# Kernel optimization log

Measured on AMD Instinct MI355X. Metric: run time of the kernel, lower is better.

The kernel has to match this reference:

```python
import jax, jax.numpy as jnp
import numpy as np

N, D, T, P, NP, H = 200000, 128, 8, 2000, 9, 2048


def setup_inputs() -> dict:
    key = jax.random.key(0)
    ks = jax.random.split(key, 12)
    inp = {
        'motion_z': jax.random.normal(ks[0], (N, D), jnp.float32),
        'tasks': jax.random.randint(ks[1], (N,), 0, T, jnp.int32),
        'tasks_mask': jax.random.randint(ks[2], (N,), 0, 2, jnp.int32),
        'patient_ids': jax.random.randint(ks[3], (N,), 0, P, jnp.int32),
        'phenos': jax.random.uniform(ks[4], (N, NP), jnp.float32),
        'phenos_mask': jax.random.randint(ks[5], (N,), 0, 2, jnp.int32),
        'W1': jax.random.normal(ks[6], (T * D, H), jnp.float32) * 0.02,
        'b1': jnp.zeros((H,), jnp.float32),
        'W2': jax.random.normal(ks[7], (H, H), jnp.float32) * 0.02,
        'b2': jnp.zeros((H,), jnp.float32),
        'W3': jax.random.normal(ks[8], (H, NP), jnp.float32) * 0.02,
        'b3': jnp.zeros((NP,), jnp.float32),
    }
    return inp


def _fingerprint(motion_z, tasks, tasks_mask, patient_ids, phenos, phenos_mask):
    # valid sample mask (tasks_mask==1 & patient id present & phenos_mask==1)
    valid = (tasks_mask == 1) & (phenos_mask == 1)
    w = valid.astype(motion_z.dtype)                      # [N]
    wz = motion_z * w[:, None]                            # [N, D]

    # global per-task mean (fallback for empty patient-task cells)
    t_sum = jax.ops.segment_sum(wz, tasks, num_segments=T)           # [T, D]
    t_cnt = jax.ops.segment_sum(w, tasks, num_segments=T)            # [T]
    task_mean = t_sum / jnp.maximum(t_cnt, 1.0)[:, None]             # [T, D]

    # fused (patient, task) segment mean — single pass scatter-reduce
    seg = patient_ids * T + tasks                                    # [N]
    pt_sum = jax.ops.segment_sum(wz, seg, num_segments=P * T)        # [P*T, D]
    pt_cnt = jax.ops.segment_sum(w, seg, num_segments=P * T)         # [P*T]
    pt_mean = pt_sum / jnp.maximum(pt_cnt, 1.0)[:, None]
    pt_mean = jnp.where((pt_cnt > 0)[:, None], pt_mean,
                        jnp.tile(task_mean, (P, 1)))                 # fallback
    fingerprint = pt_mean.reshape(P, T * D)

    # first valid pheno row per patient (phenos_id_each[0])
    idxs = jnp.where(valid, jnp.arange(N), N)
    first = jnp.full((P,), N, jnp.int32).at[patient_ids].min(idxs.astype(jnp.int32))
    uni_phenos = phenos[jnp.clip(first, 0, N - 1)]                   # [P, NP]
    return fingerprint, uni_phenos


def reference(motion_z, tasks, tasks_mask, patient_ids, phenos, phenos_mask,
              W1, b1, W2, b2, W3, b3):
    fingerprint, uni_phenos = _fingerprint(
        motion_z, tasks, tasks_mask, patient_ids, phenos, phenos_mask)
    h = jax.nn.relu(fingerprint @ W1 + b1)
    h = jax.nn.relu(h @ W2 + b2)
    pheno_latent = h @ W3 + b3
    out = jax.nn.sigmoid(pheno_latent)
    return out, uni_phenos, pheno_latent
```

## Files before the change

### kernel.cpp

```cpp
#include <hip/hip_runtime.h>
#include <math.h>

#define N_SAMP 200000
#define D_     128
#define T_     8
#define P_     2000
#define NP_    9
#define H_     2048
#define MPAD   2048

#define OFF_PTSUM   0
#define SZ_PTSUM    (16000*128*4)
#define OFF_PTCNT   8192000
#define SZ_PTCNT    (16000*4)
#define OFF_FIRST   8256000
#define SZ_FIRST    (P_*4)
#define OFF_TMEAN   8264192
#define OFF_FPHI    8268288
#define OFF_FPLO    12462592
#define OFF_W1THI   16656896
#define OFF_W1TLO   20851200
#define OFF_H1HI    25045504
#define OFF_H1LO    33434112
#define OFF_W2THI   41822720
#define OFF_W2TLO   50211328
#define OFF_H2      OFF_FPHI
#define OFF_TSUM    OFF_H1HI
#define OFF_TCNT    (OFF_H1HI + 4096)

typedef __attribute__((ext_vector_type(8))) short bf16x8;
typedef __attribute__((ext_vector_type(4))) float f32x4;

__device__ __forceinline__ unsigned f2bf_rne(float x) {
    unsigned b = __float_as_uint(x);
    return (b + 0x7fffu + ((b >> 16) & 1u)) >> 16;
}
__device__ __forceinline__ float bf2f(unsigned u) {
    return __uint_as_float(u << 16);
}

__device__ __forceinline__ void gload16(const void* g, void* l) {
    __builtin_amdgcn_global_load_lds(
        (const __attribute__((address_space(1))) unsigned int*)g,
        (__attribute__((address_space(3))) unsigned int*)l, 16, 0, 0);
}

__global__ __launch_bounds__(256) void scatter_pt(
    const float* __restrict__ motion_z, const int* __restrict__ tasks,
    const int* __restrict__ tmask, const int* __restrict__ pids,
    const int* __restrict__ pmask, float* __restrict__ pt_sum,
    float* __restrict__ pt_cnt, int* __restrict__ first)
{
    int wid0 = (blockIdx.x * blockDim.x + threadIdx.x) >> 6;
    int lane = threadIdx.x & 63;
    int nw   = (gridDim.x * blockDim.x) >> 6;
    for (int wid = wid0; wid < N_SAMP; wid += nw) {
        if (tmask[wid] != 1 || pmask[wid] != 1) continue;
        int seg = pids[wid] * T_ + tasks[wid];
        if (lane == 0) {
            atomicAdd(&pt_cnt[seg], 1.0f);
            atomicMin(&first[pids[wid]], wid);
        }
        float2 v = *(const float2*)&motion_z[(size_t)wid * D_ + lane * 2];
        atomicAdd(&pt_sum[seg * D_ + lane * 2 + 0], v.x);
        atomicAdd(&pt_sum[seg * D_ + lane * 2 + 1], v.y);
    }
}

__global__ __launch_bounds__(256) void tsum_partial(
    const float* __restrict__ pt_sum, const float* __restrict__ pt_cnt,
    float* __restrict__ tsum, float* __restrict__ tcnt)
{
    int p0 = blockIdx.x * 16;
    int tid = threadIdx.x;
    float4 acc = make_float4(0.f, 0.f, 0.f, 0.f);
    for (int pl = 0; pl < 16; ++pl) {
        float4 v = *(const float4*)&pt_sum[(size_t)(p0 + pl) * 1024 + tid * 4];
        acc.x += v.x; acc.y += v.y; acc.z += v.z; acc.w += v.w;
    }
    atomicAdd(&tsum[tid * 4 + 0], acc.x);
    atomicAdd(&tsum[tid * 4 + 1], acc.y);
    atomicAdd(&tsum[tid * 4 + 2], acc.z);
    atomicAdd(&tsum[tid * 4 + 3], acc.w);
    if (tid < 128) {
        int p = p0 + (tid >> 3), t = tid & 7;
        atomicAdd(&tcnt[t], pt_cnt[p * 8 + t]);
    }
}

__global__ __launch_bounds__(256) void tmean_div(
    const float* __restrict__ tsum, const float* __restrict__ tcnt,
    float* __restrict__ tmean)
{
    int e = blockIdx.x * 256 + threadIdx.x;
    if (e >= 1024) return;
    tmean[e] = tsum[e] / fmaxf(tcnt[e >> 7], 1.0f);
}

__global__ __launch_bounds__(256) void finalize_split(
    const float* __restrict__ pt_sum, const float* __restrict__ pt_cnt,
    const float* __restrict__ tmean,
    unsigned short* __restrict__ fphi, unsigned short* __restrict__ fplo)
{
    int e = blockIdx.x * blockDim.x + threadIdx.x;
    int p = e >> 10, col = e & 1023;
    float v = 0.f;
    if (p < P_) {
        int seg = p * T_ + (col >> 7);
        float c = pt_cnt[seg];
        v = (c > 0.f) ? pt_sum[e] / c : tmean[col];
    }
    unsigned hi = f2bf_rne(v);
    float lo = v - bf2f(hi);
    fphi[e] = (unsigned short)hi;
    fplo[e] = (unsigned short)f2bf_rne(lo);
}

__global__ void gather_phenos(const int* __restrict__ first,
                              const float* __restrict__ phenos,
                              float* __restrict__ up)
{
    int e = blockIdx.x * blockDim.x + threadIdx.x;
    if (e >= P_ * NP_) return;
    int p = e / NP_, j = e - p * NP_;
    int idx = first[p];
    if (idx > N_SAMP - 1) idx = N_SAMP - 1;
    up[e] = phenos[(size_t)idx * NP_ + j];
}

__global__ __launch_bounds__(256) void conv_w_t(
    const float* __restrict__ W, unsigned short* __restrict__ Whi,
    unsigned short* __restrict__ Wlo, int K, int N)
{
    __shared__ float tile[32][36];
    int k0 = blockIdx.y * 32, n0 = blockIdx.x * 32;
    int r = threadIdx.x >> 3, c4 = (threadIdx.x & 7) * 4;
    float4 v = *(const float4*)&W[(size_t)(k0 + r) * N + n0 + c4];
    tile[r][c4 + 0] = v.x; tile[r][c4 + 1] = v.y;
    tile[r][c4 + 2] = v.z; tile[r][c4 + 3] = v.w;
    __syncthreads();
    unsigned short hi[4], lo[4];
#pragma unroll
    for (int q = 0; q < 4; ++q) {
        float x = tile[c4 + q][r];
        unsigned h = f2bf_rne(x);
        hi[q] = (unsigned short)h;
        lo[q] = (unsigned short)f2bf_rne(x - bf2f(h));
    }
    size_t o = (size_t)(n0 + r) * K + k0 + c4;
    *(ushort4*)&Whi[o] = make_ushort4(hi[0], hi[1], hi[2], hi[3]);
    *(ushort4*)&Wlo[o] = make_ushort4(lo[0], lo[1], lo[2], lo[3]);
}

template<int OUTF32>
__global__ __launch_bounds__(256, 1) void gemm_split(
    const unsigned short* __restrict__ Ahi, const unsigned short* __restrict__ Alo,
    const unsigned short* __restrict__ Bhi, const unsigned short* __restrict__ Blo,
    const float* __restrict__ bias,
    float* __restrict__ Cf, unsigned short* __restrict__ Chi,
    unsigned short* __restrict__ Clo, int K)
{
    __shared__ __align__(16) char lds[2][4][8192];
    int tid  = threadIdx.x;
    int lane = tid & 63, w = tid >> 6;
    int wr = w >> 1, wc = w & 1;
    int row0 = blockIdx.y * 128, col0 = blockIdx.x * 128;

    int fr = lane & 15;
    int fk = (lane >> 4) * 8;

    const unsigned short* srcs[4] = {Ahi, Alo, Bhi, Blo};
    int base0[4] = {row0, row0, col0, col0};

    auto STAGE = [&](int buf, int t) {
        int k0 = t * 32;
#pragma unroll
        for (int pc = 0; pc < 4; ++pc) {
#pragma unroll
            for (int rep = 0; rep < 2; ++rep) {
                int tile = rep * 4 + w;
                const unsigned short* g =
                    srcs[pc] + (size_t)(base0[pc] + tile * 16 + fr) * K + k0 + fk;
                gload16(g, &lds[buf][pc][tile * 1024]);
            }
        }
    };

    f32x4 acc[4][4] = {};
    int nt = K / 32;
    STAGE(0, 0);
    __syncthreads();
    int cur = 0;
    int lo16 = lane * 16;

    for (int t = 0; t < nt; ++t) {
        if (t + 1 < nt) STAGE(cur ^ 1, t + 1);
        bf16x8 ah[4], al[4], bh[4], bl[4];
#pragma unroll
        for (int i = 0; i < 4; ++i) {
            ah[i] = *(const bf16x8*)&lds[cur][0][(wr * 4 + i) * 1024 + lo16];
            al[i] = *(const bf16x8*)&lds[cur][1][(wr * 4 + i) * 1024 + lo16];
        }
#pragma unroll
        for (int j = 0; j < 4; ++j) {
            bh[j] = *(const bf16x8*)&lds[cur][2][(wc * 4 + j) * 1024 + lo16];
            bl[j] = *(const bf16x8*)&lds[cur][3][(wc * 4 + j) * 1024 + lo16];
        }
#pragma unroll
        for (int i = 0; i < 4; ++i)
#pragma unroll
            for (int j = 0; j < 4; ++j) {
                acc[i][j] = __builtin_amdgcn_mfma_f32_16x16x32_bf16(ah[i], bh[j], acc[i][j], 0, 0, 0);
                acc[i][j] = __builtin_amdgcn_mfma_f32_16x16x32_bf16(ah[i], bl[j], acc[i][j], 0, 0, 0);
                acc[i][j] = __builtin_amdgcn_mfma_f32_16x16x32_bf16(al[i], bh[j], acc[i][j], 0, 0, 0);
            }
        __syncthreads();
        cur ^= 1;
    }

#pragma unroll
    for (int i = 0; i < 4; ++i) {
        int r = row0 + wr * 64 + i * 16 + (lane >> 4) * 4;
#pragma unroll
        for (int j = 0; j < 4; ++j) {
            int c = col0 + wc * 64 + j * 16 + (lane & 15);
            float bv = bias[c];
#pragma unroll
            for (int q = 0; q < 4; ++q) {
                float x = fmaxf(acc[i][j][q] + bv, 0.f);
                size_t o = (size_t)(r + q) * H_ + c;
                if (OUTF32) {
                    Cf[o] = x;
                } else {
                    unsigned hb = f2bf_rne(x);
                    Chi[o] = (unsigned short)hb;
                    Clo[o] = (unsigned short)f2bf_rne(x - bf2f(hb));
                }
            }
        }
    }
}

__global__ __launch_bounds__(256) void out_head(
    const float* __restrict__ h2, const float* __restrict__ W3,
    const float* __restrict__ b3, float* __restrict__ out,
    float* __restrict__ latent)
{
    int wid  = (blockIdx.x * blockDim.x + threadIdx.x) >> 6;
    int lane = threadIdx.x & 63;
    if (wid >= P_) return;
    const float* hrow = h2 + (size_t)wid * H_;
    float acc[NP_] = {};
    for (int k = lane; k < H_; k += 64) {
        float h = hrow[k];
        const float* wr = W3 + (size_t)k * NP_;
#pragma unroll
        for (int j = 0; j < NP_; ++j) acc[j] = fmaf(h, wr[j], acc[j]);
    }
#pragma unroll
    for (int off = 32; off > 0; off >>= 1)
#pragma unroll
        for (int j = 0; j < NP_; ++j) acc[j] += __shfl_down(acc[j], off);
    if (lane == 0) {
#pragma unroll
        for (int j = 0; j < NP_; ++j) {
            float v = acc[j] + b3[j];
            latent[wid * NP_ + j] = v;
            out[wid * NP_ + j]    = 1.f / (1.f + expf(-v));
        }
    }
}

extern "C" void kernel_launch(void* const* d_in, const int* in_sizes, int n_in,
                              void* d_out, int out_size, void* d_ws, size_t ws_size,
                              hipStream_t stream)
{
    const float* motion_z = (const float*)d_in[0];
    const int*   tasks    = (const int*)d_in[1];
    const int*   tmask    = (const int*)d_in[2];
    const int*   pids     = (const int*)d_in[3];
    const float* phenos   = (const float*)d_in[4];
    const int*   pmask    = (const int*)d_in[5];
    const float* W1 = (const float*)d_in[6];
    const float* b1 = (const float*)d_in[7];
    const float* W2 = (const float*)d_in[8];
    const float* b2 = (const float*)d_in[9];
    const float* W3 = (const float*)d_in[10];
    const float* b3 = (const float*)d_in[11];

    char* ws = (char*)d_ws;
    float*          pt_sum = (float*)(ws + OFF_PTSUM);
    float*          pt_cnt = (float*)(ws + OFF_PTCNT);
    int*            first  = (int*)  (ws + OFF_FIRST);
    float*          tmean  = (float*)(ws + OFF_TMEAN);
    float*          tsum   = (float*)(ws + OFF_TSUM);
    float*          tcnt   = (float*)(ws + OFF_TCNT);
    unsigned short* fphi   = (unsigned short*)(ws + OFF_FPHI);
    unsigned short* fplo   = (unsigned short*)(ws + OFF_FPLO);
    unsigned short* w1thi  = (unsigned short*)(ws + OFF_W1THI);
    unsigned short* w1tlo  = (unsigned short*)(ws + OFF_W1TLO);
    unsigned short* h1hi   = (unsigned short*)(ws + OFF_H1HI);
    unsigned short* h1lo   = (unsigned short*)(ws + OFF_H1LO);
    unsigned short* w2thi  = (unsigned short*)(ws + OFF_W2THI);
    unsigned short* w2tlo  = (unsigned short*)(ws + OFF_W2TLO);
    float*          h2     = (float*)(ws + OFF_H2);

    float* out    = (float*)d_out;
    float* uni    = out + P_ * NP_;
    float* latent = out + 2 * P_ * NP_;

    hipMemsetAsync(pt_sum, 0,    SZ_PTSUM, stream);
    hipMemsetAsync(pt_cnt, 0,    SZ_PTCNT, stream);
    hipMemsetAsync(first,  0x7f, SZ_FIRST, stream);
    hipMemsetAsync(tsum,   0,    4096 + 256, stream);

    scatter_pt<<<2048, 256, 0, stream>>>(motion_z, tasks, tmask, pids,
                                         pmask, pt_sum, pt_cnt, first);
    tsum_partial<<<125, 256, 0, stream>>>(pt_sum, pt_cnt, tsum, tcnt);
    tmean_div<<<4, 256, 0, stream>>>(tsum, tcnt, tmean);
    finalize_split<<<(MPAD * 1024) / 256, 256, 0, stream>>>(
        pt_sum, pt_cnt, tmean, fphi, fplo);
    gather_phenos<<<(P_ * NP_ + 255) / 256, 256, 0, stream>>>(first, phenos, uni);

    conv_w_t<<<dim3(H_ / 32, 1024 / 32), 256, 0, stream>>>(W1, w1thi, w1tlo, 1024, H_);
    conv_w_t<<<dim3(H_ / 32, H_ / 32),   256, 0, stream>>>(W2, w2thi, w2tlo, H_, H_);

    gemm_split<0><<<dim3(H_ / 128, MPAD / 128), 256, 0, stream>>>(
        fphi, fplo, w1thi, w1tlo, b1, nullptr, h1hi, h1lo, 1024);
    gemm_split<1><<<dim3(H_ / 128, MPAD / 128), 256, 0, stream>>>(
        h1hi, h1lo, w2thi, w2tlo, b2, h2, nullptr, nullptr, H_);

    out_head<<<P_ / 4, 256, 0, stream>>>(h2, W3, b3, out, latent);
}
```

Baseline: 447.8 us.

## Replace atomic scatter with counting-sort gather for patient-task segment sums

Replaces the float atomicAdd scatter of motion_z into patient-task cells with a histogram, a single-block exclusive scan, an index scatter into a permutation, and a per-cell wavefront gather that sums rows without atomics and writes pt_sum directly. The aim is to remove heavy float atomic contention and the large pt_sum memset. It also merges the pheno gather into the task-mean kernel, stages W3 in LDS for the output head, and changes the conv_w_t tile padding. The cost is extra kernel launches, a serial one-block scan, and irregular gather reads through perm.

```diff
diff --git a/kernel.cpp b/kernel.cpp
--- a/kernel.cpp
+++ b/kernel.cpp
@@ -8,25 +8,27 @@
 #define NP_    9
 #define H_     2048
 #define MPAD   2048
-
-#define OFF_PTSUM   0
-#define SZ_PTSUM    (16000*128*4)
-#define OFF_PTCNT   8192000
-#define SZ_PTCNT    (16000*4)
-#define OFF_FIRST   8256000
-#define SZ_FIRST    (P_*4)
-#define OFF_TMEAN   8264192
-#define OFF_FPHI    8268288
-#define OFF_FPLO    12462592
-#define OFF_W1THI   16656896
-#define OFF_W1TLO   20851200
-#define OFF_H1HI    25045504
-#define OFF_H1LO    33434112
-#define OFF_W2THI   41822720
-#define OFF_W2TLO   50211328
+#define NSEG   16000
+#define NSEGP  16384
+
+#define OFF_CNT     0
+#define OFF_CURSOR  65536
+#define OFF_OFFS    131072
+#define OFF_FIRST   196608
+#define OFF_PERM    204800
+#define OFF_TMEAN   1004800
+#define OFF_TSUM    1008896
+#define OFF_TCNT    1012992
+#define OFF_PTSUM   1013760
+#define OFF_FPHI    9205760
+#define OFF_FPLO    13400064
+#define OFF_W1THI   17594368
+#define OFF_W1TLO   21788672
+#define OFF_H1HI    25982976
+#define OFF_H1LO    34371584
+#define OFF_W2THI   42760192
+#define OFF_W2TLO   51148800
 #define OFF_H2      OFF_FPHI
-#define OFF_TSUM    OFF_H1HI
-#define OFF_TCNT    (OFF_H1HI + 4096)
 
 typedef __attribute__((ext_vector_type(8))) short bf16x8;
 typedef __attribute__((ext_vector_type(4))) float f32x4;
@@ -45,30 +47,77 @@
         (__attribute__((address_space(3))) unsigned int*)l, 16, 0, 0);
 }
 
-__global__ __launch_bounds__(256) void scatter_pt(
-    const float* __restrict__ motion_z, const int* __restrict__ tasks,
-    const int* __restrict__ tmask, const int* __restrict__ pids,
-    const int* __restrict__ pmask, float* __restrict__ pt_sum,
-    float* __restrict__ pt_cnt, int* __restrict__ first)
-{
-    int wid0 = (blockIdx.x * blockDim.x + threadIdx.x) >> 6;
+__global__ __launch_bounds__(256) void hist_first(
+    const int* __restrict__ tasks, const int* __restrict__ tmask,
+    const int* __restrict__ pids, const int* __restrict__ pmask,
+    int* __restrict__ cnt, int* __restrict__ first)
+{
+    int i = blockIdx.x * 256 + threadIdx.x;
+    if (i >= N_SAMP) return;
+    if (tmask[i] != 1 || pmask[i] != 1) return;
+    int p = pids[i];
+    atomicAdd(&cnt[p * T_ + tasks[i]], 1);
+    atomicMin(&first[p], i);
+}
+
+__global__ __launch_bounds__(256) void scan16k(
+    const int* __restrict__ cnt, int* __restrict__ offs)
+{
+    __shared__ int part[256];
+    int tid = threadIdx.x;
+    int base = tid * 64;
+    int s = 0;
+#pragma unroll 8
+    for (int j = 0; j < 64; ++j) s += cnt[base + j];
+    part[tid] = s;
+    __syncthreads();
+    for (int d = 1; d < 256; d <<= 1) {
+        int v = (tid >= d) ? part[tid - d] : 0;
+        __syncthreads();
+        part[tid] += v;
+        __syncthreads();
+    }
+    int run = (tid > 0) ? part[tid - 1] : 0;
+    for (int j = 0; j < 64; ++j) {
+        offs[base + j] = run;
+        run += cnt[base + j];
+    }
+}
+
+__global__ __launch_bounds__(256) void scatter_idx(
+    const int* __restrict__ tasks, const int* __restrict__ tmask,
+    const int* __restrict__ pids, const int* __restrict__ pmask,
+    const int* __restrict__ offs, int* __restrict__ cursor,
+    int* __restrict__ perm)
+{
+    int i = blockIdx.x * 256 + threadIdx.x;
+    if (i >= N_SAMP) return;
+    if (tmask[i] != 1 || pmask[i] != 1) return;
+    int seg = pids[i] * T_ + tasks[i];
+    int pos = atomicAdd(&cursor[seg], 1);
+    perm[offs[seg] + pos] = i;
+}
+
+__global__ __launch_bounds__(256) void gather_cell(
+    const float* __restrict__ motion_z, const int* __restrict__ cnt,
+    const int* __restrict__ offs, const int* __restrict__ perm,
+    float* __restrict__ pt_sum)
+{
+    int wid  = (blockIdx.x * 256 + threadIdx.x) >> 6;
     int lane = threadIdx.x & 63;
-    int nw   = (gridDim.x * blockDim.x) >> 6;
-    for (int wid = wid0; wid < N_SAMP; wid += nw) {
-        if (tmask[wid] != 1 || pmask[wid] != 1) continue;
-        int seg = pids[wid] * T_ + tasks[wid];
-        if (lane == 0) {
-            atomicAdd(&pt_cnt[seg], 1.0f);
-            atomicMin(&first[pids[wid]], wid);
-        }
-        float2 v = *(const float2*)&motion_z[(size_t)wid * D_ + lane * 2];
-        atomicAdd(&pt_sum[seg * D_ + lane * 2 + 0], v.x);
-        atomicAdd(&pt_sum[seg * D_ + lane * 2 + 1], v.y);
-    }
+    if (wid >= NSEG) return;
+    int c = cnt[wid], base = offs[wid];
+    float2 acc = make_float2(0.f, 0.f);
+    for (int r = 0; r < c; ++r) {
+        int idx = perm[base + r];
+        float2 v = *(const float2*)&motion_z[(size_t)idx * D_ + lane * 2];
+        acc.x += v.x; acc.y += v.y;
+    }
+    *(float2*)&pt_sum[(size_t)wid * D_ + lane * 2] = acc;
 }
 
 __global__ __launch_bounds__(256) void tsum_partial(
-    const float* __restrict__ pt_sum, const float* __restrict__ pt_cnt,
+    const float* __restrict__ pt_sum, const int* __restrict__ cnt,
     float* __restrict__ tsum, float* __restrict__ tcnt)
 {
     int p0 = blockIdx.x * 16;
@@ -84,21 +133,31 @@
     atomicAdd(&tsum[tid * 4 + 3], acc.w);
     if (tid < 128) {
         int p = p0 + (tid >> 3), t = tid & 7;
-        atomicAdd(&tcnt[t], pt_cnt[p * 8 + t]);
-    }
-}
-
-__global__ __launch_bounds__(256) void tmean_div(
+        atomicAdd(&tcnt[t], (float)cnt[p * 8 + t]);
+    }
+}
+
+__global__ __launch_bounds__(256) void tmean_gather(
     const float* __restrict__ tsum, const float* __restrict__ tcnt,
-    float* __restrict__ tmean)
+    float* __restrict__ tmean, const int* __restrict__ first,
+    const float* __restrict__ phenos, float* __restrict__ up)
 {
     int e = blockIdx.x * 256 + threadIdx.x;
-    if (e >= 1024) return;
-    tmean[e] = tsum[e] / fmaxf(tcnt[e >> 7], 1.0f);
+    if (e < 1024) {
+        tmean[e] = tsum[e] / fmaxf(tcnt[e >> 7], 1.0f);
+    } else {
+        int g = e - 1024;
+        if (g < P_ * NP_) {
+            int p = g / NP_, j = g - p * NP_;
+            int idx = first[p];
+            if (idx > N_SAMP - 1) idx = N_SAMP - 1;
+            up[g] = phenos[(size_t)idx * NP_ + j];
+        }
+    }
 }
 
 __global__ __launch_bounds__(256) void finalize_split(
-    const float* __restrict__ pt_sum, const float* __restrict__ pt_cnt,
+    const float* __restrict__ pt_sum, const int* __restrict__ cnt,
     const float* __restrict__ tmean,
     unsigned short* __restrict__ fphi, unsigned short* __restrict__ fplo)
 {
@@ -107,8 +166,8 @@
     float v = 0.f;
     if (p < P_) {
         int seg = p * T_ + (col >> 7);
-        float c = pt_cnt[seg];
-        v = (c > 0.f) ? pt_sum[e] / c : tmean[col];
+        int c = cnt[seg];
+        v = (c > 0) ? pt_sum[e] / (float)c : tmean[col];
     }
     unsigned hi = f2bf_rne(v);
     float lo = v - bf2f(hi);
@@ -116,23 +175,11 @@
     fplo[e] = (unsigned short)f2bf_rne(lo);
 }
 
-__global__ void gather_phenos(const int* __restrict__ first,
-                              const float* __restrict__ phenos,
-                              float* __restrict__ up)
-{
-    int e = blockIdx.x * blockDim.x + threadIdx.x;
-    if (e >= P_ * NP_) return;
-    int p = e / NP_, j = e - p * NP_;
-    int idx = first[p];
-    if (idx > N_SAMP - 1) idx = N_SAMP - 1;
-    up[e] = phenos[(size_t)idx * NP_ + j];
-}
-
 __global__ __launch_bounds__(256) void conv_w_t(
     const float* __restrict__ W, unsigned short* __restrict__ Whi,
     unsigned short* __restrict__ Wlo, int K, int N)
 {
-    __shared__ float tile[32][36];
+    __shared__ float tile[32][33];
     int k0 = blockIdx.y * 32, n0 = blockIdx.x * 32;
     int r = threadIdx.x >> 3, c4 = (threadIdx.x & 7) * 4;
     float4 v = *(const float4*)&W[(size_t)(k0 + r) * N + n0 + c4];
@@ -246,16 +293,21 @@
     const float* __restrict__ b3, float* __restrict__ out,
     float* __restrict__ latent)
 {
-    int wid  = (blockIdx.x * blockDim.x + threadIdx.x) >> 6;
-    int lane = threadIdx.x & 63;
+    __shared__ float w3s[H_ * NP_];
+    int tid = threadIdx.x;
+    for (int e = tid * 4; e < H_ * NP_; e += 1024)
+        *(float4*)&w3s[e] = *(const float4*)&W3[e];
+    __syncthreads();
+
+    int wid  = blockIdx.x * 4 + (tid >> 6);
+    int lane = tid & 63;
     if (wid >= P_) return;
     const float* hrow = h2 + (size_t)wid * H_;
     float acc[NP_] = {};
     for (int k = lane; k < H_; k += 64) {
         float h = hrow[k];
-        const float* wr = W3 + (size_t)k * NP_;
-#pragma unroll
-        for (int j = 0; j < NP_; ++j) acc[j] = fmaf(h, wr[j], acc[j]);
+#pragma unroll
+        for (int j = 0; j < NP_; ++j) acc[j] = fmaf(h, w3s[k * NP_ + j], acc[j]);
     }
 #pragma unroll
     for (int off = 32; off > 0; off >>= 1)
@@ -289,12 +341,15 @@
     const float* b3 = (const float*)d_in[11];
 
     char* ws = (char*)d_ws;
-    float*          pt_sum = (float*)(ws + OFF_PTSUM);
-    float*          pt_cnt = (float*)(ws + OFF_PTCNT);
+    int*            cnt    = (int*)  (ws + OFF_CNT);
+    int*            cursor = (int*)  (ws + OFF_CURSOR);
+    int*            offs   = (int*)  (ws + OFF_OFFS);
     int*            first  = (int*)  (ws + OFF_FIRST);
+    int*            perm   = (int*)  (ws + OFF_PERM);
     float*          tmean  = (float*)(ws + OFF_TMEAN);
     float*          tsum   = (float*)(ws + OFF_TSUM);
     float*          tcnt   = (float*)(ws + OFF_TCNT);
+    float*          pt_sum = (float*)(ws + OFF_PTSUM);
     unsigned short* fphi   = (unsigned short*)(ws + OFF_FPHI);
     unsigned short* fplo   = (unsigned short*)(ws + OFF_FPLO);
     unsigned short* w1thi  = (unsigned short*)(ws + OFF_W1THI);
@@ -309,18 +364,22 @@
     float* uni    = out + P_ * NP_;
     float* latent = out + 2 * P_ * NP_;
 
-    hipMemsetAsync(pt_sum, 0,    SZ_PTSUM, stream);
-    hipMemsetAsync(pt_cnt, 0,    SZ_PTCNT, stream);
-    hipMemsetAsync(first,  0x7f, SZ_FIRST, stream);
-    hipMemsetAsync(tsum,   0,    4096 + 256, stream);
-
-    scatter_pt<<<2048, 256, 0, stream>>>(motion_z, tasks, tmask, pids,
-                                         pmask, pt_sum, pt_cnt, first);
-    tsum_partial<<<125, 256, 0, stream>>>(pt_sum, pt_cnt, tsum, tcnt);
-    tmean_div<<<4, 256, 0, stream>>>(tsum, tcnt, tmean);
+    hipMemsetAsync(cnt,   0,    2 * NSEGP * 4, stream);
+    hipMemsetAsync(first, 0x7f, P_ * 4, stream);
+    hipMemsetAsync(tsum,  0,    4096 + 256, stream);
+
+    int nrb = (N_SAMP + 255) / 256;
+    hist_first<<<nrb, 256, 0, stream>>>(tasks, tmask, pids, pmask, cnt, first);
+    scan16k<<<1, 256, 0, stream>>>(cnt, offs);
+    scatter_idx<<<nrb, 256, 0, stream>>>(tasks, tmask, pids, pmask, offs,
+                                         cursor, perm);
+    gather_cell<<<(NSEG * 64 + 255) / 256, 256, 0, stream>>>(
+        motion_z, cnt, offs, perm, pt_sum);
+    tsum_partial<<<125, 256, 0, stream>>>(pt_sum, cnt, tsum, tcnt);
+    tmean_gather<<<(1024 + P_ * NP_ + 255) / 256, 256, 0, stream>>>(
+        tsum, tcnt, tmean, first, phenos, uni);
     finalize_split<<<(MPAD * 1024) / 256, 256, 0, stream>>>(
-        pt_sum, pt_cnt, tmean, fphi, fplo);
-    gather_phenos<<<(P_ * NP_ + 255) / 256, 256, 0, stream>>>(first, phenos, uni);
+        pt_sum, cnt, tmean, fphi, fplo);
 
     conv_w_t<<<dim3(H_ / 32, 1024 / 32), 256, 0, stream>>>(W1, w1thi, w1tlo, 1024, H_);
     conv_w_t<<<dim3(H_ / 32, H_ / 32),   256, 0, stream>>>(W2, w2thi, w2tlo, H_, H_);
```

Result: faster. 425.0 us (-5.1%).
